# Optimization experiments

Hardware: AMD Instinct MI355X
Metric: run time of the kernel (lower is better)

## Reference

```python
import jax, jax.numpy as jnp
import numpy as np

EMBED_DIM = 1024
NUM_HEADS = 8
HEAD_DIM = EMBED_DIM // NUM_HEADS  # 128
MAX_DIST = 128
RADIUS = 256
R = 2 * MAX_DIST + 1  # 257 relative-position embeddings


def setup_inputs() -> dict:
    key = jax.random.key(0)
    ks = jax.random.split(key, 8)
    B, Sq, Sk = 4, 1024, 1024
    s = 0.02
    return {
        "Q": jax.random.normal(ks[0], (B, Sq, EMBED_DIM), jnp.float32),
        "K": jax.random.normal(ks[1], (B, Sk, EMBED_DIM), jnp.float32),
        "V": jax.random.normal(ks[2], (B, Sk, EMBED_DIM), jnp.float32),
        "segment_ids": jnp.zeros((B, Sq), jnp.int32),
        "key_padding_mask": jnp.zeros((B, Sk), jnp.bool_),
        "Wq": jax.random.normal(ks[3], (EMBED_DIM, EMBED_DIM), jnp.float32) * s,
        "Wk": jax.random.normal(ks[4], (EMBED_DIM, EMBED_DIM), jnp.float32) * s,
        "Wv": jax.random.normal(ks[5], (EMBED_DIM, EMBED_DIM), jnp.float32) * s,
        "Wo": jax.random.normal(ks[6], (EMBED_DIM, EMBED_DIM), jnp.float32) * s,
        "rel_emb": jax.random.normal(ks[7], (NUM_HEADS, R, HEAD_DIM), jnp.float32) * s,
    }


def _proj(x, W, B, S):
    # Linear (no bias) then split heads: (B,S,d) -> (B*h, S, head_dim)
    y = x @ W.T
    return y.reshape(B, S, NUM_HEADS, HEAD_DIM).transpose(0, 2, 1, 3).reshape(B * NUM_HEADS, S, HEAD_DIM)


def _attention(Q, K, V, key_padding_mask, Wq, Wk, Wv, Wo, rel_emb):
    B, Sq, _ = Q.shape
    Sk = K.shape[1]
    Qp = _proj(Q, Wq, B, Sq)
    Kp = _proj(K, Wk, B, Sk)
    Vp = _proj(V, Wv, B, Sk)

    iq = jnp.arange(Sq)
    ik = jnp.arange(Sk)
    # clipped relative offsets -> bias table indices, shape (Sq, Sk)
    rel_ids = jnp.clip(ik[None, :] - iq[:, None], -MAX_DIST, MAX_DIST) + MAX_DIST

    # per-head table tiled over batch: (B*h, R, head_dim)
    rel_embeds = jnp.broadcast_to(rel_emb[None], (B, NUM_HEADS, R, HEAD_DIM)).reshape(B * NUM_HEADS, R, HEAD_DIM)

    Q_rel = jnp.einsum('bqd,brd->bqr', Qp, rel_embeds)        # (B*h, Sq, R)
    energy = jnp.einsum('bqd,bkd->bqk', Qp, Kp)               # (B*h, Sq, Sk)
    rel_shift = Q_rel[:, iq[:, None], rel_ids]                # gather along R -> (B*h, Sq, Sk)
    energy = (energy + rel_shift) / jnp.sqrt(jnp.float32(HEAD_DIM))

    local_mask = jnp.abs(ik[None, :] - iq[:, None]) > RADIUS  # (Sq, Sk) slided band
    mask = local_mask[None, None] | key_padding_mask[:, None, None, :]  # (B,1,Sq,Sk)
    mask = jnp.broadcast_to(mask, (B, NUM_HEADS, Sq, Sk)).reshape(B * NUM_HEADS, Sq, Sk)
    energy = jnp.where(mask, -jnp.inf, energy)

    attn = jax.nn.softmax(energy, axis=2)
    out = jnp.matmul(attn, Vp)                                # (B*h, Sq, head_dim)
    # permute(0,2,3,1): head_dim-major then head, matching the torch module
    out = out.reshape(B, NUM_HEADS, Sq, HEAD_DIM).transpose(0, 2, 3, 1).reshape(B, Sq, HEAD_DIM * NUM_HEADS)
    return out @ Wo.T


def reference(Q, K, V, segment_ids, key_padding_mask, Wq, Wk, Wv, Wo, rel_emb):
    # segment_ids is unused by the 'slided' RPE variant
    return _attention(Q, K, V, key_padding_mask, Wq, Wk, Wv, Wo, rel_emb)
```

## Files before the change

kernel.cpp:

```cpp
#include <hip/hip_runtime.h>

typedef __attribute__((ext_vector_type(8))) short short8;
typedef __attribute__((ext_vector_type(4))) short short4v;
typedef __attribute__((ext_vector_type(4))) float float4a;
typedef __attribute__((ext_vector_type(16))) float float16a;
typedef __attribute__((ext_vector_type(4))) unsigned int uint4v;

#define MFMA16(a, b, c) __builtin_amdgcn_mfma_f32_16x16x32_bf16(a, b, c, 0, 0, 0)
#define MFMA32(a, b, c) __builtin_amdgcn_mfma_f32_32x32x16_bf16(a, b, c, 0, 0, 0)

static __device__ __forceinline__ short f2bf(float f) {
  unsigned u = __builtin_bit_cast(unsigned, f);
  u += 0x7fff + ((u >> 16) & 1);
  return (short)(u >> 16);
}
static __device__ __forceinline__ float bf2f(short s) {
  unsigned u = ((unsigned)(unsigned short)s) << 16;
  return __builtin_bit_cast(float, u);
}

static __device__ __forceinline__ void gl2lds(const short* g, short* l) {
  __builtin_amdgcn_global_load_lds(
      (const __attribute__((address_space(1))) void*)g,
      (__attribute__((address_space(3))) void*)l,
      16, 0, 0);
}

struct Cvt8 { const float* in[8]; short* out[8]; };
__global__ __launch_bounds__(256) void cvt8_k(Cvt8 a) {
  int b = blockIdx.x, seg, rb;
  if (b < 12288)      { seg = b >> 12;                 rb = b & 4095; }
  else if (b < 16384) { seg = 3 + ((b - 12288) >> 10); rb = (b - 12288) & 1023; }
  else                { seg = 7;                       rb = b - 16384; }
  int i = rb * 256 + threadIdx.x;
  if (seg == 6) {
    int o = i * 4;
    int n = o >> 10, kp = o & 1023;
    int h = kp >> 7, d0 = kp & 127;
    const float* src = a.in[6] + n * 1024 + h;
    short4v s;
    s.x = f2bf(src[d0 * 8]);
    s.y = f2bf(src[d0 * 8 + 8]);
    s.z = f2bf(src[d0 * 8 + 16]);
    s.w = f2bf(src[d0 * 8 + 24]);
    ((short4v*)a.out[6])[i] = s;
    return;
  }
  float4a v = ((const float4a*)a.in[seg])[i];
  short4v o;
  o.x = f2bf(v.x); o.y = f2bf(v.y); o.z = f2bf(v.z); o.w = f2bf(v.w);
  ((short4v*)a.out[seg])[i] = o;
}

__global__ __launch_bounds__(256) void gemm_qkv(
    const short* __restrict__ Qb, const short* __restrict__ Kb, const short* __restrict__ Vb,
    const short* __restrict__ Wq, const short* __restrict__ Wk, const short* __restrict__ Wv,
    short* __restrict__ Qp, short* __restrict__ Kp, short* __restrict__ Vt) {
  __shared__ short pool[32768];
  int bid = blockIdx.x;
  int xcd = bid & 7, slot = bid >> 3;
  int seg = slot >> 5, r = slot & 31;
  int mt = ((xcd >> 1) << 3) | (r >> 2);
  int nt = ((xcd & 1) << 2) | (r & 3);
  const short* A = seg == 0 ? Qb : (seg == 1 ? Kb : Vb);
  const short* W = seg == 0 ? Wq : (seg == 1 ? Wk : Wv);
  int m0 = mt * 128, n0 = nt * 128;
  int tid = threadIdx.x;
  int lane = tid & 63, wid = tid >> 6;
  int l15 = lane & 15, quad = lane >> 4;
  int wm = wid & 1, wn = wid >> 1;

  int srow = lane >> 3, sunit = (lane & 7) ^ (lane >> 3);
  const short* gA = A + (m0 + wid * 32 + srow) * 1024 + sunit * 8;
  const short* gB = W + (n0 + wid * 32 + srow) * 1024 + sunit * 8;
  int stoff = (wid * 32) * 64;
  int sw = l15 & 7;

  float4a acc[4][4];
#pragma unroll
  for (int i = 0; i < 4; ++i)
#pragma unroll
    for (int j = 0; j < 4; ++j) acc[i][j] = (float4a){0, 0, 0, 0};

#pragma unroll
  for (int t = 0; t < 4; ++t) {
    gl2lds(gA + t * 8192, pool + stoff + t * 512);
    gl2lds(gB + t * 8192, pool + 8192 + stoff + t * 512);
  }
  __syncthreads();

  int cur = 0;
  for (int kc = 0; kc < 1024; kc += 64) {
    if (kc < 960) {
      short* nxt = pool + ((cur ^ 1) << 14);
#pragma unroll
      for (int t = 0; t < 4; ++t) {
        gl2lds(gA + kc + 64 + t * 8192, nxt + stoff + t * 512);
        gl2lds(gB + kc + 64 + t * 8192, nxt + 8192 + stoff + t * 512);
      }
    }
    const short* As = pool + (cur << 14);
    const short* Bs = As + 8192;
#pragma unroll
    for (int ks = 0; ks < 2; ++ks) {
      short8 af[4], bfr[4];
#pragma unroll
      for (int i = 0; i < 4; ++i)
        af[i] = *(const short8*)&As[(wm * 64 + i * 16 + l15) * 64 +
                                    (((ks * 4 + quad) ^ sw) * 8)];
#pragma unroll
      for (int j = 0; j < 4; ++j)
        bfr[j] = *(const short8*)&Bs[(wn * 64 + j * 16 + l15) * 64 +
                                     (((ks * 4 + quad) ^ sw) * 8)];
#pragma unroll
      for (int i = 0; i < 4; ++i)
#pragma unroll
        for (int j = 0; j < 4; ++j) acc[i][j] = MFMA16(af[i], bfr[j], acc[i][j]);
    }
    __syncthreads();
    cur ^= 1;
  }

  if (seg < 2) {
    float scl = (seg == 0) ? 0.12752745707470575f : 1.0f;
#pragma unroll
    for (int i = 0; i < 4; ++i)
#pragma unroll
      for (int j = 0; j < 4; ++j)
#pragma unroll
        for (int r2 = 0; r2 < 4; ++r2) {
          int m = m0 + wm * 64 + i * 16 + quad * 4 + r2;
          int n = n0 + wn * 64 + j * 16 + l15;
          int bb = m >> 10, s = m & 1023, hh = n >> 7, d = n & 127;
          short v = f2bf(acc[i][j][r2] * scl);
          if (seg == 0) Qp[(((bb * 8 + hh) * 1024) + s) * 128 + d] = v;
          else          Kp[(((bb * 8 + hh) * 1024) + s) * 128 + d] = v;
        }
  } else {
    short* T = pool;
    int b2 = m0 >> 10, s0 = m0 & 1023;
    long vb2 = (long)(b2 * 8 + nt) * 131072;
#pragma unroll
    for (int hd = 0; hd < 2; ++hd) {
      __syncthreads();
      if (wn == hd) {
#pragma unroll
        for (int j = 0; j < 4; ++j)
#pragma unroll
          for (int i = 0; i < 4; ++i)
#pragma unroll
            for (int r2 = 0; r2 < 4; ++r2)
              T[(j * 16 + l15) * 132 + wm * 64 + i * 16 + quad * 4 + r2] =
                  f2bf(acc[i][j][r2]);
      }
      __syncthreads();
#pragma unroll
      for (int rr = 0; rr < 4; ++rr) {
        int d = rr * 16 + (tid >> 4);
        short8 v = *(const short8*)&T[d * 132 + (tid & 15) * 8];
        *(short8*)&Vt[vb2 + (hd * 64 + d) * 1024 + s0 + (tid & 15) * 8] = v;
      }
    }
  }
}

__global__ __launch_bounds__(256) void gemm_o(const short* __restrict__ A,
                                              const short* __restrict__ W,
                                              float* __restrict__ C) {
  __shared__ short pool[24576];
  int bid = blockIdx.x;
  int xcd = bid & 7, slot = bid >> 3;
  int mt = ((xcd >> 1) << 3) | (slot >> 3);
  int nt = ((xcd & 1) << 3) | (slot & 7);
  int m0 = mt * 128, n0 = nt * 64;
  int lane = threadIdx.x & 63, wid = threadIdx.x >> 6;
  int l15 = lane & 15, quad = lane >> 4;
  int wm = wid & 1, wn = wid >> 1;

  int srow = lane >> 3, sunit = (lane & 7) ^ (lane >> 3);
  int bb = m0 >> 10, q0t = m0 & 1023;
  const short* gA = A + bb * 1048576 + (q0t + wid * 32 + srow) * 128 + sunit * 8;
  const short* gB = W + (n0 + wid * 16 + srow) * 1024 + sunit * 8;
  int saoff = (wid * 32) * 64;
  int sboff = (wid * 16) * 64;
  int sw = l15 & 7;

  float4a acc[4][2];
#pragma unroll
  for (int i = 0; i < 4; ++i)
#pragma unroll
    for (int j = 0; j < 2; ++j) acc[i][j] = (float4a){0, 0, 0, 0};

#pragma unroll
  for (int t = 0; t < 4; ++t) gl2lds(gA + t * 1024, pool + saoff + t * 512);
#pragma unroll
  for (int t = 0; t < 2; ++t) gl2lds(gB + t * 8192, pool + 8192 + sboff + t * 512);
  __syncthreads();

  int cur = 0;
  for (int kc = 0; kc < 1024; kc += 64) {
    if (kc < 960) {
      int kn = kc + 64;
      int koff = (kn >> 7) * 131072 + (kn & 64);
      short* nxt = pool + ((cur ^ 1) * 12288);
#pragma unroll
      for (int t = 0; t < 4; ++t) gl2lds(gA + koff + t * 1024, nxt + saoff + t * 512);
#pragma unroll
      for (int t = 0; t < 2; ++t) gl2lds(gB + kn + t * 8192, nxt + 8192 + sboff + t * 512);
    }
    const short* As = pool + cur * 12288;
    const short* Bs = As + 8192;
#pragma unroll
    for (int ks = 0; ks < 2; ++ks) {
      short8 af[4], bfr[2];
#pragma unroll
      for (int i = 0; i < 4; ++i)
        af[i] = *(const short8*)&As[(wm * 64 + i * 16 + l15) * 64 +
                                    (((ks * 4 + quad) ^ sw) * 8)];
#pragma unroll
      for (int j = 0; j < 2; ++j)
        bfr[j] = *(const short8*)&Bs[(wn * 32 + j * 16 + l15) * 64 +
                                     (((ks * 4 + quad) ^ sw) * 8)];
#pragma unroll
      for (int i = 0; i < 4; ++i)
#pragma unroll
        for (int j = 0; j < 2; ++j) acc[i][j] = MFMA16(af[i], bfr[j], acc[i][j]);
    }
    __syncthreads();
    cur ^= 1;
  }

#pragma unroll
  for (int i = 0; i < 4; ++i)
#pragma unroll
    for (int j = 0; j < 2; ++j)
#pragma unroll
      for (int r2 = 0; r2 < 4; ++r2) {
        int m = m0 + wm * 64 + i * 16 + quad * 4 + r2;
        int n = n0 + wn * 32 + j * 16 + l15;
        C[m * 1024 + n] = acc[i][j][r2];
      }
}

__global__ __launch_bounds__(256) void qrel_k(const short* __restrict__ Qp,
                                              const short* __restrict__ rel,
                                              short* __restrict__ Qrel) {
  int lane = threadIdx.x & 63, wid = threadIdx.x >> 6;
  int bid = blockIdx.x;
  int xcd = bid & 7, slot = bid >> 3;
  int bh = (xcd << 2) | (slot & 3);
  int mtg = slot >> 2;
  int mt = mtg * 4 + wid;
  int l15 = lane & 15, quad = lane >> 4;
  int h = bh & 7;

  const short* arow = Qp + bh * 131072 + (mt * 16 + l15) * 128 + quad * 8;
  short8 a[4];
#pragma unroll
  for (int t = 0; t < 4; ++t) a[t] = *(const short8*)(arow + t * 32);

  const short* rbase = rel + h * 32896 + quad * 8;
  for (int nt = 0; nt < 17; ++nt) {
    int col = nt * 16 + l15;
    int colc = col > 256 ? 256 : col;
    const short* brow = rbase + colc * 128;
    float4a acc = {0, 0, 0, 0};
#pragma unroll
    for (int t = 0; t < 4; ++t) {
      short8 b = *(const short8*)(brow + t * 32);
      acc = MFMA16(a[t], b, acc);
    }
    if (col < 257) {
#pragma unroll
      for (int r = 0; r < 4; ++r) {
        int q = mt * 16 + quad * 4 + r;
        Qrel[bh * 264192 + q * 258 + col] = f2bf(acc[r]);
      }
    }
  }
}

__global__ __launch_bounds__(256, 2) void attn_k(const short* __restrict__ Qp,
                                                 const short* __restrict__ Kp,
                                                 const short* __restrict__ Vt,
                                                 const short* __restrict__ Qrel,
                                                 const unsigned char* __restrict__ kpm,
                                                 short* __restrict__ O2) {
  __shared__ __align__(16) short pool[32896];
  short* qlds = pool;
  short* Kbuf = pool + 16512;
  short* Vbuf = pool + 16512 + 8192;
  float* obuf = (float*)(pool + 16512);
  float* lbuf = (float*)pool;
  int tid = threadIdx.x;
  int lane = tid & 63, wid = tid >> 6;
  int qt = wid & 1, kh = wid >> 1;
  int bid = blockIdx.x;
  int bh = ((bid & 7) << 2) | ((bid >> 3) & 3);
  int qsb = bid >> 5;
  int Q0 = qsb * 64;
  int q0 = Q0 + qt * 32;
  int l31 = lane & 31, hl = lane >> 5;
  int b = bh >> 3;

  int klo = Q0 - 256; if (klo < 0) klo = 0;
  int khi = Q0 + 320; if (khi > 1024) khi = 1024;

  const short* kgbase = Kp + (long)bh * 131072;
  const short* vgbase = Vt + (long)bh * 131072;
  const unsigned char* pmrow = kpm + b * 1024;

  int ksr = lane >> 4, ksu = lane & 15;
  int vsr = lane >> 3, vsu = (lane & 7) ^ (lane >> 3);

#define STAGE_KV(KT)                                                          \
  {                                                                           \
    int _k0 = (KT);                                                           \
    _Pragma("unroll")                                                         \
    for (int c = 0; c < 4; ++c) {                                             \
      int rl = wid * 16 + c * 4 + ksr;                                        \
      gl2lds(kgbase + (long)(_k0 + rl) * 128 + ((ksu ^ (c * 4 + ksr)) * 8),   \
             Kbuf + (wid * 16 + c * 4) * 128);                                \
    }                                                                         \
    _Pragma("unroll")                                                         \
    for (int c = 0; c < 4; ++c) {                                             \
      int rl = wid * 32 + c * 8 + vsr;                                        \
      gl2lds(vgbase + (long)rl * 1024 + _k0 + vsu * 8,                        \
             Vbuf + (wid * 32 + c * 8) * 64);                                 \
    }                                                                         \
  }

  {
    const short8* src = (const short8*)(Qrel + bh * 264192 + Q0 * 258);
    short8* dst = (short8*)qlds;
    for (int i = tid; i < 2064; i += 256) dst[i] = src[i];
  }
  short8 aq[8];
  const short* qrow = Qp + bh * 131072 + (q0 + l31) * 128 + hl * 8;
#pragma unroll
  for (int s = 0; s < 8; ++s) aq[s] = *(const short8*)(qrow + s * 16);
  STAGE_KV(klo);
  unsigned char pmb = pmrow[klo + kh * 32 + l31];
  __syncthreads();
  unsigned pm32 = (unsigned)__ballot(pmb != 0);

  float16a O[4];
#pragma unroll
  for (int d = 0; d < 4; ++d)
#pragma unroll
    for (int i = 0; i < 16; ++i) O[d][i] = 0.f;
  float lsum = 0.f;

  int qv = q0 + l31;
  int rowb = (qt * 32 + l31) * 258;
  int r15 = l31 & 15;
  int d7 = l31 & 7;

  for (int k0 = klo; k0 < khi; k0 += 64) {
    int kw = k0 + kh * 32;
    short8 kf[8];
    const short* Kr = Kbuf + (kh * 32 + l31) * 128;
#pragma unroll
    for (int s = 0; s < 8; ++s)
      kf[s] = *(const short8*)&Kr[(((2 * s + hl) ^ r15) * 8)];
    short8 vf0[4], vf1[4];
#pragma unroll
    for (int dblk = 0; dblk < 4; ++dblk) {
      const short* Vr = Vbuf + (dblk * 32 + l31) * 64;
      vf0[dblk] = *(const short8*)&Vr[(((kh * 4 + hl) ^ d7) * 8)];
      vf1[dblk] = *(const short8*)&Vr[(((kh * 4 + 2 + hl) ^ d7) * 8)];
    }
    __syncthreads();

    int k1 = k0 + 64;
    unsigned char pmn = 0;
    if (k1 < khi) {
      STAGE_KV(k1);
      pmn = pmrow[k1 + kh * 32 + l31];
    }
    unsigned pmc = pm32;

    float16a S;
#pragma unroll
    for (int i = 0; i < 16; ++i) S[i] = 0.f;
#pragma unroll
    for (int s = 0; s < 8; ++s) S = MFMA32(kf[s], aq[s], S);

    int dq = kw - qv;
    bool edge = (kw - q0 < -224) | (kw - q0 > 224) | (pmc != 0);
    if (!edge) {
      int rb = dq + 4 * hl + 128;
#pragma unroll
      for (int i = 0; i < 16; ++i) {
        int rr = rb + (i & 3) + 8 * (i >> 2);
        rr = rr < 0 ? 0 : (rr > 256 ? 256 : rr);
        float pe = __builtin_amdgcn_exp2f(S[i] + bf2f(qlds[rowb + rr]));
        S[i] = pe;
        lsum += pe;
      }
    } else {
#pragma unroll
      for (int i = 0; i < 16; ++i) {
        int koff = (i & 3) + 8 * (i >> 2) + 4 * hl;
        int dd = dq + koff;
        int rr = dd < -128 ? 0 : (dd > 128 ? 256 : dd + 128);
        float rel = bf2f(qlds[rowb + rr]);
        int msk = (dd < -256) | (dd > 256) | (int)((pmc >> koff) & 1u);
        float pe = msk ? 0.f : __builtin_amdgcn_exp2f(S[i] + rel);
        S[i] = pe;
        lsum += pe;
      }
    }

    short8 ap0, ap1;
    {
      unsigned x0, y0, z0, w0;
      asm("v_cvt_pk_bf16_f32 %0, %1, %2" : "=v"(x0) : "v"(S[0]), "v"(S[1]));
      asm("v_cvt_pk_bf16_f32 %0, %1, %2" : "=v"(y0) : "v"(S[2]), "v"(S[3]));
      asm("v_cvt_pk_bf16_f32 %0, %1, %2" : "=v"(z0) : "v"(S[4]), "v"(S[5]));
      asm("v_cvt_pk_bf16_f32 %0, %1, %2" : "=v"(w0) : "v"(S[6]), "v"(S[7]));
      asm("v_permlane32_swap_b32 %0, %1" : "+v"(x0), "+v"(z0));
      asm("v_permlane32_swap_b32 %0, %1" : "+v"(y0), "+v"(w0));
      uint4v u0 = {x0, y0, z0, w0};
      ap0 = __builtin_bit_cast(short8, u0);
      unsigned x1, y1, z1, w1;
      asm("v_cvt_pk_bf16_f32 %0, %1, %2" : "=v"(x1) : "v"(S[8]), "v"(S[9]));
      asm("v_cvt_pk_bf16_f32 %0, %1, %2" : "=v"(y1) : "v"(S[10]), "v"(S[11]));
      asm("v_cvt_pk_bf16_f32 %0, %1, %2" : "=v"(z1) : "v"(S[12]), "v"(S[13]));
      asm("v_cvt_pk_bf16_f32 %0, %1, %2" : "=v"(w1) : "v"(S[14]), "v"(S[15]));
      asm("v_permlane32_swap_b32 %0, %1" : "+v"(x1), "+v"(z1));
      asm("v_permlane32_swap_b32 %0, %1" : "+v"(y1), "+v"(w1));
      uint4v u1 = {x1, y1, z1, w1};
      ap1 = __builtin_bit_cast(short8, u1);
    }

#pragma unroll
    for (int dblk = 0; dblk < 4; ++dblk) {
      O[dblk] = MFMA32(ap0, vf0[dblk], O[dblk]);
      O[dblk] = MFMA32(ap1, vf1[dblk], O[dblk]);
    }

    __syncthreads();
    pm32 = (unsigned)__ballot(pmn != 0);
  }
#undef STAGE_KV

  lsum += __shfl_xor(lsum, 32);
  __syncthreads();
  if (kh == 1) {
    if (hl == 0) lbuf[qt * 32 + l31] = lsum;
#pragma unroll
    for (int dblk = 0; dblk < 4; ++dblk)
#pragma unroll
      for (int i = 0; i < 16; ++i) {
        int qoff = (i & 3) + 8 * (i >> 2) + 4 * hl;
        obuf[(qt * 32 + qoff) * 128 + dblk * 32 + l31] = O[dblk][i];
      }
  }
  __syncthreads();
  if (kh == 0) {
    if (hl == 0) {
      float inv = __builtin_amdgcn_rcpf(lsum + lbuf[qt * 32 + l31]);
      lbuf[qt * 32 + l31] = inv;
    }
#pragma unroll
    for (int dblk = 0; dblk < 4; ++dblk)
#pragma unroll
      for (int i = 0; i < 16; ++i) {
        int qoff = (i & 3) + 8 * (i >> 2) + 4 * hl;
        obuf[(qt * 32 + qoff) * 128 + dblk * 32 + l31] += O[dblk][i];
      }
  }
  __syncthreads();

#pragma unroll
  for (int it = 0; it < 4; ++it) {
    int idx = tid + it * 256;
    int q = idx >> 4, d = (idx & 15) * 8;
    float inv = lbuf[q];
    const float* ob = &obuf[q * 128 + d];
    short8 v;
#pragma unroll
    for (int j = 0; j < 8; ++j) v[j] = f2bf(ob[j] * inv);
    *(short8*)&O2[(long)bh * 131072 + (long)(Q0 + q) * 128 + d] = v;
  }
}

extern "C" void kernel_launch(void* const* d_in, const int* in_sizes, int n_in,
                              void* d_out, int out_size, void* d_ws, size_t ws_size,
                              hipStream_t stream) {
  const float* Q   = (const float*)d_in[0];
  const float* K   = (const float*)d_in[1];
  const float* V   = (const float*)d_in[2];
  const unsigned char* kpm = (const unsigned char*)d_in[4];
  const float* Wq  = (const float*)d_in[5];
  const float* Wk  = (const float*)d_in[6];
  const float* Wv  = (const float*)d_in[7];
  const float* Wo  = (const float*)d_in[8];
  const float* rel = (const float*)d_in[9];
  float* out = (float*)d_out;

  short* ws = (short*)d_ws;
  short* Qb   = ws;
  short* Kb   = Qb + 4194304;
  short* Vb   = Kb + 4194304;
  short* Wqb  = Vb + 4194304;
  short* Wkb  = Wqb + 1048576;
  short* Wvb  = Wkb + 1048576;
  short* Wob  = Wvb + 1048576;
  short* relb = Wob + 1048576;
  short* Qp   = relb + 263168;
  short* Kp   = Qp + 4194304;
  short* Vt   = Kp + 4194304;
  short* O2   = Vt + 4194304;
  short* Qrel = Qb;

  Cvt8 ca;
  ca.in[0] = Q;  ca.out[0] = Qb;
  ca.in[1] = K;  ca.out[1] = Kb;
  ca.in[2] = V;  ca.out[2] = Vb;
  ca.in[3] = Wq; ca.out[3] = Wqb;
  ca.in[4] = Wk; ca.out[4] = Wkb;
  ca.in[5] = Wv; ca.out[5] = Wvb;
  ca.in[6] = Wo; ca.out[6] = Wob;
  ca.in[7] = rel; ca.out[7] = relb;
  cvt8_k<<<dim3(16641), dim3(256), 0, stream>>>(ca);

  gemm_qkv<<<dim3(768), dim3(256), 0, stream>>>(Qb, Kb, Vb, Wqb, Wkb, Wvb, Qp, Kp, Vt);
  qrel_k<<<dim3(512), dim3(256), 0, stream>>>(Qp, relb, Qrel);
  attn_k<<<dim3(512), dim3(256), 0, stream>>>(Qp, Kp, Vt, Qrel, kpm, O2);
  gemm_o<<<dim3(512), dim3(256), 0, stream>>>(O2, Wob, out);
}
```

Baseline: 210.9 us.

## Fuse Q-relative-position matmul into QKV projection epilogue

Removes the separate qrel_k launch and computes Q·rel_emb inside the gemm_qkv epilogue for the Q segment. The 128x128 bf16 Q tile is staged through LDS and multiplied against the head's 257-entry table with MFMA. This avoids re-reading Qp from global memory and one kernel launch. In exchange, the Q-segment blocks do extra serial work, which can unbalance the 768-block grid. Qrel also moves to its own workspace region because Qb is still being read while it is written.

```diff
diff --git a/kernel.cpp b/kernel.cpp
--- a/kernel.cpp
+++ b/kernel.cpp
@@ -55,6 +55,7 @@
 __global__ __launch_bounds__(256) void gemm_qkv(
     const short* __restrict__ Qb, const short* __restrict__ Kb, const short* __restrict__ Vb,
     const short* __restrict__ Wq, const short* __restrict__ Wk, const short* __restrict__ Wv,
+    const short* __restrict__ Rel, short* __restrict__ Qrel,
     short* __restrict__ Qp, short* __restrict__ Kp, short* __restrict__ Vt) {
   __shared__ short pool[32768];
   int bid = blockIdx.x;
@@ -136,6 +137,47 @@
           if (seg == 0) Qp[(((bb * 8 + hh) * 1024) + s) * 128 + d] = v;
           else          Kp[(((bb * 8 + hh) * 1024) + s) * 128 + d] = v;
         }
+    if (seg == 0) {
+      short* T2 = pool;
+#pragma unroll
+      for (int i = 0; i < 4; ++i)
+#pragma unroll
+        for (int j = 0; j < 4; ++j)
+#pragma unroll
+          for (int r2 = 0; r2 < 4; ++r2)
+            T2[(wm * 64 + i * 16 + quad * 4 + r2) * 132 + wn * 64 + j * 16 + l15] =
+                f2bf(acc[i][j][r2] * scl);
+      __syncthreads();
+      int h = nt;
+      int b3 = m0 >> 10, s0 = m0 & 1023;
+      long qbase = (long)(b3 * 8 + h) * 264192;
+      const short* rbase = Rel + h * 32896 + quad * 8;
+#pragma unroll
+      for (int half = 0; half < 2; ++half) {
+        int w8 = wid + half * 4;
+        const short* arow2 = T2 + (w8 * 16 + l15) * 132 + quad * 8;
+        short8 a2[4];
+#pragma unroll
+        for (int t = 0; t < 4; ++t) a2[t] = *(const short8*)(arow2 + t * 32);
+        for (int ntc = 0; ntc < 17; ++ntc) {
+          int col = ntc * 16 + l15;
+          int colc = col > 256 ? 256 : col;
+          const short* brow = rbase + colc * 128;
+          float4a acq = {0, 0, 0, 0};
+#pragma unroll
+          for (int t = 0; t < 4; ++t) {
+            short8 bq = *(const short8*)(brow + t * 32);
+            acq = MFMA16(a2[t], bq, acq);
+          }
+          if (col < 257) {
+#pragma unroll
+            for (int r2 = 0; r2 < 4; ++r2)
+              Qrel[qbase + (long)(s0 + w8 * 16 + quad * 4 + r2) * 258 + col] =
+                  f2bf(acq[r2]);
+          }
+        }
+      }
+    }
   } else {
     short* T = pool;
     int b2 = m0 >> 10, s0 = m0 & 1023;
@@ -240,44 +282,6 @@
         int n = n0 + wn * 32 + j * 16 + l15;
         C[m * 1024 + n] = acc[i][j][r2];
       }
-}
-
-__global__ __launch_bounds__(256) void qrel_k(const short* __restrict__ Qp,
-                                              const short* __restrict__ rel,
-                                              short* __restrict__ Qrel) {
-  int lane = threadIdx.x & 63, wid = threadIdx.x >> 6;
-  int bid = blockIdx.x;
-  int xcd = bid & 7, slot = bid >> 3;
-  int bh = (xcd << 2) | (slot & 3);
-  int mtg = slot >> 2;
-  int mt = mtg * 4 + wid;
-  int l15 = lane & 15, quad = lane >> 4;
-  int h = bh & 7;
-
-  const short* arow = Qp + bh * 131072 + (mt * 16 + l15) * 128 + quad * 8;
-  short8 a[4];
-#pragma unroll
-  for (int t = 0; t < 4; ++t) a[t] = *(const short8*)(arow + t * 32);
-
-  const short* rbase = rel + h * 32896 + quad * 8;
-  for (int nt = 0; nt < 17; ++nt) {
-    int col = nt * 16 + l15;
-    int colc = col > 256 ? 256 : col;
-    const short* brow = rbase + colc * 128;
-    float4a acc = {0, 0, 0, 0};
-#pragma unroll
-    for (int t = 0; t < 4; ++t) {
-      short8 b = *(const short8*)(brow + t * 32);
-      acc = MFMA16(a[t], b, acc);
-    }
-    if (col < 257) {
-#pragma unroll
-      for (int r = 0; r < 4; ++r) {
-        int q = mt * 16 + quad * 4 + r;
-        Qrel[bh * 264192 + q * 258 + col] = f2bf(acc[r]);
-      }
-    }
-  }
 }
 
 __global__ __launch_bounds__(256, 2) void attn_k(const short* __restrict__ Qp,
@@ -331,7 +335,7 @@
   }
 
   {
-    const short8* src = (const short8*)(Qrel + bh * 264192 + Q0 * 258);
+    const short8* src = (const short8*)(Qrel + (long)bh * 264192 + Q0 * 258);
     short8* dst = (short8*)qlds;
     for (int i = tid; i < 2064; i += 256) dst[i] = src[i];
   }
@@ -513,7 +517,7 @@
   short* Kp   = Qp + 4194304;
   short* Vt   = Kp + 4194304;
   short* O2   = Vt + 4194304;
-  short* Qrel = Qb;
+  short* Qrel = O2 + 4194304;
 
   Cvt8 ca;
   ca.in[0] = Q;  ca.out[0] = Qb;
@@ -526,8 +530,8 @@
   ca.in[7] = rel; ca.out[7] = relb;
   cvt8_k<<<dim3(16641), dim3(256), 0, stream>>>(ca);
 
-  gemm_qkv<<<dim3(768), dim3(256), 0, stream>>>(Qb, Kb, Vb, Wqb, Wkb, Wvb, Qp, Kp, Vt);
-  qrel_k<<<dim3(512), dim3(256), 0, stream>>>(Qp, relb, Qrel);
+  gemm_qkv<<<dim3(768), dim3(256), 0, stream>>>(Qb, Kb, Vb, Wqb, Wkb, Wvb,
+                                                relb, Qrel, Qp, Kp, Vt);
   attn_k<<<dim3(512), dim3(256), 0, stream>>>(Qp, Kp, Vt, Qrel, kpm, O2);
   gemm_o<<<dim3(512), dim3(256), 0, stream>>>(O2, Wob, out);
 }
```

Result: faster. 202.6 us (-3.9%).
